# Kernel optimization log

Measured on AMD Instinct MI355X. Metric: run time of the kernel, lower is better.

## Reference

```python
import jax, jax.numpy as jnp
import numpy as np

EMBED_DIM = 1024
B, S = 8, 2048


def setup_inputs() -> dict:
    key = jax.random.key(0)
    ks = jax.random.split(key, 9)
    d = EMBED_DIM
    scale = 1.0 / np.sqrt(d)
    return {
        "x": jax.random.normal(ks[0], (B, S, d), dtype=jnp.float32),
        "Wq": jax.random.normal(ks[1], (d, d), dtype=jnp.float32) * scale,
        "bq": jnp.zeros((d,), dtype=jnp.float32),
        "Wk": jax.random.normal(ks[2], (d, d), dtype=jnp.float32) * scale,
        "bk": jnp.zeros((d,), dtype=jnp.float32),
        "Wv": jax.random.normal(ks[3], (d, d), dtype=jnp.float32) * scale,
        "bv": jnp.zeros((d,), dtype=jnp.float32),
        "ln_gamma": jnp.ones((d,), dtype=jnp.float32),
        "ln_beta": jnp.zeros((d,), dtype=jnp.float32),
    }


def _layernorm(x, gamma, beta, eps=1e-5):
    mu = jnp.mean(x, axis=-1, keepdims=True)
    var = jnp.var(x, axis=-1, keepdims=True)
    return (x - mu) * jax.lax.rsqrt(var + eps) * gamma + beta


def reference(x, Wq, bq, Wk, bk, Wv, bv, ln_gamma, ln_beta):
    # Pre-LN single-head self-attention with residual.
    # Dropout is identity (eval mode) for a deterministic reference.
    residual = x
    xn = _layernorm(x, ln_gamma, ln_beta)
    Q = jnp.einsum('bsd,de->bse', xn, Wq.T) + bq  # torch Linear: x @ W^T + b
    K = jnp.einsum('bsd,de->bse', xn, Wk.T) + bk
    V = jnp.einsum('bsd,de->bse', xn, Wv.T) + bv
    scores = jnp.einsum('bqd,bkd->bqk', Q, K) / jnp.sqrt(jnp.float32(EMBED_DIM))
    attention_weights = jax.nn.softmax(scores, axis=-1)  # [B, S, S]
    attention_output = jnp.einsum('bqk,bkd->bqd', attention_weights, V)
    output = residual + attention_output
    return (output, attention_weights)
```

## Files before the change

### kernel.cpp

```cpp
#include <hip/hip_runtime.h>

#define EMBED 1024
#define SEQ 2048
#define BATCH 8

typedef __bf16 bf16;
typedef bf16 bf16x4 __attribute__((ext_vector_type(4)));
typedef bf16 bf16x8 __attribute__((ext_vector_type(8)));
typedef float f32x4 __attribute__((ext_vector_type(4)));

__device__ __forceinline__ void async_copy16(const bf16* g, bf16* l) {
  __builtin_amdgcn_global_load_lds(
      (const __attribute__((address_space(1))) unsigned int*)g,
      (__attribute__((address_space(3))) unsigned int*)l, 16, 0, 0);
}

template <int KDEPTH, int LDA, int LDB>
__device__ __forceinline__ void gemm_core(const bf16* __restrict__ Ab,
                                          const bf16* __restrict__ Bb,
                                          bf16* lds, f32x4 (&acc)[8][4]) {
  const int tid = (int)threadIdx.x;
  const int lane = tid & 63;
  const int wid = tid >> 6;
  const int wm = wid >> 2, wn = wid & 3;
  const int c = lane & 15, g = lane >> 4;
  const int sx = c & 7;
  constexpr int NT = KDEPTH / 64;

  int srow[4], scol[4];
#pragma unroll
  for (int r = 0; r < 4; ++r) {
    int idx = r * 512 + tid;
    srow[r] = idx >> 3;
    scol[r] = ((idx & 7) ^ ((idx >> 3) & 7)) * 8;
  }

  auto stage = [&](int bufsel, int t) {
    bf16* dst = lds + bufsel * 32768;
    const int k0 = t * 64;
#pragma unroll
    for (int r = 0; r < 4; ++r)
      async_copy16(Ab + (size_t)srow[r] * LDA + k0 + scol[r], dst + (r * 512 + tid) * 8);
#pragma unroll
    for (int r = 0; r < 4; ++r)
      async_copy16(Bb + (size_t)srow[r] * LDB + k0 + scol[r], dst + 16384 + (r * 512 + tid) * 8);
  };

  stage(0, 0);
  stage(1, 1);
  asm volatile("s_waitcnt vmcnt(8)" ::: "memory");
  __builtin_amdgcn_s_barrier();
  __builtin_amdgcn_sched_barrier(0);

  const int aoffb = (wm * 128 + c) * 64;
  const int boffb = (wn * 64 + c) * 64;

  for (int t = 0; t < NT; ++t) {
    const bf16* bufA = lds + (t & 1) * 32768;
    const bf16* bufB = bufA + 16384;

    bf16x8 bfr[4][2];
#pragma unroll
    for (int ni = 0; ni < 4; ++ni)
#pragma unroll
      for (int ks = 0; ks < 2; ++ks)
        bfr[ni][ks] = *reinterpret_cast<const bf16x8*>(
            bufB + boffb + ni * 1024 + (((ks * 4 + g) ^ sx) * 8));
    __builtin_amdgcn_s_setprio(1);
#pragma unroll
    for (int p = 0; p < 4; ++p) {
      bf16x8 afr[2][2];
#pragma unroll
      for (int mm = 0; mm < 2; ++mm)
#pragma unroll
        for (int ks = 0; ks < 2; ++ks)
          afr[mm][ks] = *reinterpret_cast<const bf16x8*>(
              bufA + aoffb + (p * 2 + mm) * 1024 + (((ks * 4 + g) ^ sx) * 8));
#pragma unroll
      for (int mm = 0; mm < 2; ++mm)
#pragma unroll
        for (int ni = 0; ni < 4; ++ni)
#pragma unroll
          for (int ks = 0; ks < 2; ++ks)
            acc[p * 2 + mm][ni] = __builtin_amdgcn_mfma_f32_16x16x32_bf16(
                afr[mm][ks], bfr[ni][ks], acc[p * 2 + mm][ni], 0, 0, 0);
    }
    __builtin_amdgcn_s_setprio(0);

    __builtin_amdgcn_sched_barrier(0);
    asm volatile("s_waitcnt lgkmcnt(0)" ::: "memory");
    __builtin_amdgcn_s_barrier();
    if (t + 2 < NT) {
      stage(t & 1, t + 2);
      asm volatile("s_waitcnt vmcnt(8)" ::: "memory");
    } else {
      asm volatile("s_waitcnt vmcnt(0)" ::: "memory");
    }
    __builtin_amdgcn_s_barrier();
    __builtin_amdgcn_sched_barrier(0);
  }
}

__global__ __launch_bounds__(256) void k_pre(const float* __restrict__ x,
                                             const float* __restrict__ gamma,
                                             const float* __restrict__ beta,
                                             const float* __restrict__ wq,
                                             const float* __restrict__ wk,
                                             const float* __restrict__ wv,
                                             bf16* __restrict__ xn,
                                             bf16* __restrict__ wall) {
  const int bid = (int)blockIdx.x;
  const int tid = (int)threadIdx.x;
  if (bid >= BATCH * SEQ) {
    int i4 = (bid - BATCH * SEQ) * 256 + tid;
    int m = i4 >> 18;
    int loc = i4 & 262143;
    const float* src = (m == 0) ? wq : (m == 1) ? wk : wv;
    float4 v = reinterpret_cast<const float4*>(src)[loc];
    bf16x4 o;
    o[0] = (bf16)v.x; o[1] = (bf16)v.y; o[2] = (bf16)v.z; o[3] = (bf16)v.w;
    reinterpret_cast<bf16x4*>(wall)[i4] = o;
    return;
  }
  const int row = bid;
  const float4 v = reinterpret_cast<const float4*>(x + (size_t)row * EMBED)[tid];
  float s = v.x + v.y + v.z + v.w;
  float q = v.x * v.x + v.y * v.y + v.z * v.z + v.w * v.w;
#pragma unroll
  for (int off = 1; off < 64; off <<= 1) {
    s += __shfl_xor(s, off);
    q += __shfl_xor(q, off);
  }
  __shared__ float ls[4], lq[4];
  int w = tid >> 6;
  if ((tid & 63) == 0) { ls[w] = s; lq[w] = q; }
  __syncthreads();
  s = ls[0] + ls[1] + ls[2] + ls[3];
  q = lq[0] + lq[1] + lq[2] + lq[3];
  float mean = s * (1.0f / EMBED);
  float var = q * (1.0f / EMBED) - mean * mean;
  float rstd = rsqrtf(var + 1e-5f);
  float4 gm = reinterpret_cast<const float4*>(gamma)[tid];
  float4 b = reinterpret_cast<const float4*>(beta)[tid];
  bf16x4 o;
  o[0] = (bf16)((v.x - mean) * rstd * gm.x + b.x);
  o[1] = (bf16)((v.y - mean) * rstd * gm.y + b.y);
  o[2] = (bf16)((v.z - mean) * rstd * gm.z + b.z);
  o[3] = (bf16)((v.w - mean) * rstd * gm.w + b.w);
  reinterpret_cast<bf16x4*>(xn + (size_t)row * EMBED)[tid] = o;
}

__global__ __launch_bounds__(512) void k_qkv256(const bf16* __restrict__ xn,
                                                const bf16* __restrict__ wall,
                                                const float* __restrict__ bq,
                                                const float* __restrict__ bk,
                                                const float* __restrict__ bv,
                                                bf16* __restrict__ qbuf,
                                                bf16* __restrict__ kbuf,
                                                bf16* __restrict__ vt) {
  extern __shared__ bf16 smem[];
  const int h = (int)blockIdx.x;
  const int xcd = h & 7, pos = h >> 3;
  const int z = pos >> 5;
  const int mtile = xcd * 8 + ((pos >> 2) & 7);
  const int ntile = pos & 3;
  const int tid = (int)threadIdx.x, lane = tid & 63, wid = tid >> 6;
  const int wm = wid >> 2, wn = wid & 3;
  const int cc = lane & 15, g = lane >> 4;
  const bf16* Ab = xn + (size_t)(mtile * 256) * EMBED;
  const bf16* Bb = wall + (size_t)z * EMBED * EMBED + (size_t)(ntile * 256) * EMBED;
  f32x4 acc[8][4];
#pragma unroll
  for (int i = 0; i < 8; ++i)
#pragma unroll
    for (int j = 0; j < 4; ++j) acc[i][j] = (f32x4){0.f, 0.f, 0.f, 0.f};
  gemm_core<EMBED, EMBED, EMBED>(Ab, Bb, smem, acc);

  const int c0 = ntile * 256 + wn * 64;
  const int r0 = mtile * 256 + wm * 128;
  if (z < 2) {
    bf16* o = z ? kbuf : qbuf;
    const float* bias = z ? bk : bq;
#pragma unroll
    for (int mi = 0; mi < 8; ++mi)
#pragma unroll
      for (int ni = 0; ni < 4; ++ni) {
        int col = c0 + ni * 16 + cc;
        float bb = bias[col];
#pragma unroll
        for (int j = 0; j < 4; ++j)
          o[(size_t)(r0 + mi * 16 + g * 4 + j) * EMBED + col] = (bf16)(acc[mi][ni][j] + bb);
      }
  } else {
#pragma unroll
    for (int mi = 0; mi < 8; ++mi) {
      int srow = r0 + mi * 16 + g * 4;
      int b = srow >> 11, sl = srow & (SEQ - 1);
#pragma unroll
      for (int ni = 0; ni < 4; ++ni) {
        int col = c0 + ni * 16 + cc;
        float bb = bv[col];
        bf16x4 pk;
#pragma unroll
        for (int j = 0; j < 4; ++j) pk[j] = (bf16)(acc[mi][ni][j] + bb);
        *reinterpret_cast<bf16x4*>(vt + (size_t)b * EMBED * SEQ + (size_t)col * SEQ + sl) = pk;
      }
    }
  }
}

__global__ __launch_bounds__(512) void k_scores256(const bf16* __restrict__ qm,
                                                   const bf16* __restrict__ km,
                                                   bf16* __restrict__ wbf,
                                                   float* __restrict__ partial) {
  extern __shared__ bf16 smem[];
  const int h = (int)blockIdx.x;
  const int bb = h & 7, pos = h >> 3;
  const int mtile = pos >> 3, ntile = pos & 7;
  const int tid = (int)threadIdx.x, lane = tid & 63, wid = tid >> 6;
  const int wm = wid >> 2, wn = wid & 3;
  const int cc = lane & 15, g = lane >> 4;
  const bf16* Ab = qm + (size_t)bb * SEQ * EMBED + (size_t)(mtile * 256) * EMBED;
  const bf16* Bb = km + (size_t)bb * SEQ * EMBED + (size_t)(ntile * 256) * EMBED;
  f32x4 acc[8][4];
#pragma unroll
  for (int i = 0; i < 8; ++i)
#pragma unroll
    for (int j = 0; j < 4; ++j) acc[i][j] = (f32x4){0.f, 0.f, 0.f, 0.f};
  gemm_core<EMBED, EMBED, EMBED>(Ab, Bb, smem, acc);

  float* red = (float*)smem;
  const int c0 = ntile * 256 + wn * 64;
#pragma unroll
  for (int mi = 0; mi < 8; ++mi) {
#pragma unroll
    for (int j = 0; j < 4; ++j) {
      int lrow = wm * 128 + mi * 16 + g * 4 + j;
      size_t grow = (size_t)bb * SEQ + mtile * 256 + lrow;
      float s = 0.f;
#pragma unroll
      for (int ni = 0; ni < 4; ++ni) {
        float e = __expf(acc[mi][ni][j] * 0.03125f);
        wbf[grow * SEQ + c0 + ni * 16 + cc] = (bf16)e;
        s += e;
      }
      s += __shfl_xor(s, 1);
      s += __shfl_xor(s, 2);
      s += __shfl_xor(s, 4);
      s += __shfl_xor(s, 8);
      if (cc == 0) red[lrow * 4 + wn] = s;
    }
  }
  __syncthreads();
  if (tid < 256) {
    float l = red[tid * 4 + 0] + red[tid * 4 + 1] + red[tid * 4 + 2] + red[tid * 4 + 3];
    partial[((size_t)bb * SEQ + mtile * 256 + tid) * 8 + ntile] = l;
  }
}

__global__ __launch_bounds__(256) void k_rowsum(const float* __restrict__ partial,
                                                float* __restrict__ rinv) {
  int row = blockIdx.x * 256 + threadIdx.x;
  const float* p = partial + (size_t)row * 8;
  float l = 0.f;
#pragma unroll
  for (int i = 0; i < 8; ++i) l += p[i];
  rinv[row] = 1.0f / l;
}

__global__ __launch_bounds__(512) void k_pv256(const bf16* __restrict__ wbf,
                                               const bf16* __restrict__ vt,
                                               const float* __restrict__ rinv,
                                               const float* __restrict__ xin,
                                               float* __restrict__ outp) {
  extern __shared__ bf16 smem[];
  const int h = (int)blockIdx.x;
  const int bb = h & 7, pos = h >> 3;
  const int mtile = pos >> 2, ntile = pos & 3;
  const int tid = (int)threadIdx.x, lane = tid & 63, wid = tid >> 6;
  const int wm = wid >> 2, wn = wid & 3;
  const int cc = lane & 15, g = lane >> 4;
  const bf16* Ab = wbf + (size_t)bb * SEQ * SEQ + (size_t)(mtile * 256) * SEQ;
  const bf16* Bb = vt + (size_t)bb * EMBED * SEQ + (size_t)(ntile * 256) * SEQ;
  f32x4 acc[8][4];
#pragma unroll
  for (int i = 0; i < 8; ++i)
#pragma unroll
    for (int j = 0; j < 4; ++j) acc[i][j] = (f32x4){0.f, 0.f, 0.f, 0.f};
  gemm_core<SEQ, SEQ, SEQ>(Ab, Bb, smem, acc);

  const int c0 = ntile * 256 + wn * 64;
#pragma unroll
  for (int mi = 0; mi < 8; ++mi) {
#pragma unroll
    for (int j = 0; j < 4; ++j) {
      size_t grow = (size_t)bb * SEQ + mtile * 256 + wm * 128 + mi * 16 + g * 4 + j;
      float ri = rinv[grow];
      size_t base = grow * EMBED;
#pragma unroll
      for (int ni = 0; ni < 4; ++ni) {
        size_t off = base + c0 + ni * 16 + cc;
        outp[off] = xin[off] + acc[mi][ni][j] * ri;
      }
    }
  }
}

__global__ __launch_bounds__(256) void k_norm_bf(const bf16* __restrict__ wbf,
                                                 const float* __restrict__ rinv,
                                                 float* __restrict__ attn) {
  size_t i8 = (size_t)blockIdx.x * 256 + threadIdx.x;
  int row = (int)(i8 >> 8);
  float ri = rinv[row];
  bf16x8 v = reinterpret_cast<const bf16x8*>(wbf)[i8];
  float4 lo, hi;
  lo.x = (float)v[0] * ri; lo.y = (float)v[1] * ri;
  lo.z = (float)v[2] * ri; lo.w = (float)v[3] * ri;
  hi.x = (float)v[4] * ri; hi.y = (float)v[5] * ri;
  hi.z = (float)v[6] * ri; hi.w = (float)v[7] * ri;
  reinterpret_cast<float4*>(attn)[i8 * 2] = lo;
  reinterpret_cast<float4*>(attn)[i8 * 2 + 1] = hi;
}

extern "C" void kernel_launch(void* const* d_in, const int* in_sizes, int n_in,
                              void* d_out, int out_size, void* d_ws, size_t ws_size,
                              hipStream_t stream) {
  const float* x = (const float*)d_in[0];
  const float* Wq = (const float*)d_in[1];
  const float* bq = (const float*)d_in[2];
  const float* Wk = (const float*)d_in[3];
  const float* bk = (const float*)d_in[4];
  const float* Wv = (const float*)d_in[5];
  const float* bv = (const float*)d_in[6];
  const float* gamma = (const float*)d_in[7];
  const float* beta = (const float*)d_in[8];

  float* out = (float*)d_out;
  float* attn = out + (size_t)BATCH * SEQ * EMBED;

  bf16* qbuf = (bf16*)d_out;
  bf16* kbuf = qbuf + (size_t)BATCH * SEQ * EMBED;

  bf16* xn = (bf16*)d_ws;
  bf16* wall = xn + (size_t)BATCH * SEQ * EMBED;
  bf16* wbf = (bf16*)d_ws;
  bf16* vt = (bf16*)d_ws + (size_t)BATCH * SEQ * SEQ;
  float* partial = (float*)((char*)d_ws + 100663296ull);
  float* rinv = (float*)((char*)d_ws + 100663296ull + 524288ull);

  hipFuncSetAttribute((const void*)k_qkv256, hipFuncAttributeMaxDynamicSharedMemorySize, 131072);
  hipFuncSetAttribute((const void*)k_scores256, hipFuncAttributeMaxDynamicSharedMemorySize, 131072);
  hipFuncSetAttribute((const void*)k_pv256, hipFuncAttributeMaxDynamicSharedMemorySize, 131072);

  k_pre<<<BATCH * SEQ + 3072, 256, 0, stream>>>(x, gamma, beta, Wq, Wk, Wv, xn, wall);
  k_qkv256<<<768, 512, 131072, stream>>>(xn, wall, bq, bk, bv, qbuf, kbuf, vt);
  k_scores256<<<512, 512, 131072, stream>>>(qbuf, kbuf, wbf, partial);
  k_rowsum<<<64, 256, 0, stream>>>(partial, rinv);
  k_pv256<<<256, 512, 131072, stream>>>(wbf, vt, rinv, x, out);
  k_norm_bf<<<16384, 256, 0, stream>>>(wbf, rinv, attn);
}
```

Baseline: 309.6 us.

## Switch GEMM core to triple-buffered 32-wide K tiles with one barrier

The shared GEMM core now stages K tiles of 32 instead of 64 and rotates through three LDS buffers instead of two. The copy for tile t+2 is issued at the start of each iteration, before the MFMAs, which removes one barrier per iteration. LDS use drops from 128 KB to 96 KB per block, and the three launches request less dynamic shared memory to match. In exchange there are twice as many iterations, each with less MFMA work to hide the wait and barrier overhead.

Result: slower. 326.1 us (+5.3%).

```diff
diff --git a/kernel.cpp b/kernel.cpp
--- a/kernel.cpp
+++ b/kernel.cpp
@@ -24,80 +24,82 @@
   const int wid = tid >> 6;
   const int wm = wid >> 2, wn = wid & 3;
   const int c = lane & 15, g = lane >> 4;
-  const int sx = c & 7;
-  constexpr int NT = KDEPTH / 64;
-
-  int srow[4], scol[4];
-#pragma unroll
-  for (int r = 0; r < 4; ++r) {
+  const int sx = c & 3;
+  constexpr int NT = KDEPTH / 32;
+
+  int srow[2], scol[2];
+#pragma unroll
+  for (int r = 0; r < 2; ++r) {
     int idx = r * 512 + tid;
-    srow[r] = idx >> 3;
-    scol[r] = ((idx & 7) ^ ((idx >> 3) & 7)) * 8;
+    srow[r] = idx >> 2;
+    scol[r] = ((idx & 3) ^ ((idx >> 2) & 3)) * 8;
   }
 
   auto stage = [&](int bufsel, int t) {
-    bf16* dst = lds + bufsel * 32768;
-    const int k0 = t * 64;
-#pragma unroll
-    for (int r = 0; r < 4; ++r)
+    bf16* dst = lds + bufsel * 16384;
+    const int k0 = t * 32;
+#pragma unroll
+    for (int r = 0; r < 2; ++r)
       async_copy16(Ab + (size_t)srow[r] * LDA + k0 + scol[r], dst + (r * 512 + tid) * 8);
 #pragma unroll
-    for (int r = 0; r < 4; ++r)
-      async_copy16(Bb + (size_t)srow[r] * LDB + k0 + scol[r], dst + 16384 + (r * 512 + tid) * 8);
+    for (int r = 0; r < 2; ++r)
+      async_copy16(Bb + (size_t)srow[r] * LDB + k0 + scol[r],
+                   dst + 8192 + (r * 512 + tid) * 8);
   };
 
   stage(0, 0);
   stage(1, 1);
-  asm volatile("s_waitcnt vmcnt(8)" ::: "memory");
+  asm volatile("s_waitcnt vmcnt(4)" ::: "memory");
   __builtin_amdgcn_s_barrier();
   __builtin_amdgcn_sched_barrier(0);
 
-  const int aoffb = (wm * 128 + c) * 64;
-  const int boffb = (wn * 64 + c) * 64;
-
+  const int aoffb = (wm * 128 + c) * 32;
+  const int boffb = (wn * 64 + c) * 32;
+
+  int cur = 0;
   for (int t = 0; t < NT; ++t) {
-    const bf16* bufA = lds + (t & 1) * 32768;
-    const bf16* bufB = bufA + 16384;
-
-    bf16x8 bfr[4][2];
+    const bf16* bufA = lds + cur * 16384;
+    const bf16* bufB = bufA + 8192;
+
+    if (t + 2 < NT) {
+      int nn = cur + 2;
+      if (nn >= 3) nn -= 3;
+      stage(nn, t + 2);
+    }
+    __builtin_amdgcn_sched_barrier(0);
+
+    bf16x8 bfr[4];
 #pragma unroll
     for (int ni = 0; ni < 4; ++ni)
-#pragma unroll
-      for (int ks = 0; ks < 2; ++ks)
-        bfr[ni][ks] = *reinterpret_cast<const bf16x8*>(
-            bufB + boffb + ni * 1024 + (((ks * 4 + g) ^ sx) * 8));
+      bfr[ni] = *reinterpret_cast<const bf16x8*>(
+          bufB + boffb + ni * 512 + ((g ^ sx) * 8));
     __builtin_amdgcn_s_setprio(1);
 #pragma unroll
     for (int p = 0; p < 4; ++p) {
-      bf16x8 afr[2][2];
+      bf16x8 afr[2];
 #pragma unroll
       for (int mm = 0; mm < 2; ++mm)
-#pragma unroll
-        for (int ks = 0; ks < 2; ++ks)
-          afr[mm][ks] = *reinterpret_cast<const bf16x8*>(
-              bufA + aoffb + (p * 2 + mm) * 1024 + (((ks * 4 + g) ^ sx) * 8));
+        afr[mm] = *reinterpret_cast<const bf16x8*>(
+            bufA + aoffb + (p * 2 + mm) * 512 + ((g ^ sx) * 8));
 #pragma unroll
       for (int mm = 0; mm < 2; ++mm)
 #pragma unroll
         for (int ni = 0; ni < 4; ++ni)
-#pragma unroll
-          for (int ks = 0; ks < 2; ++ks)
-            acc[p * 2 + mm][ni] = __builtin_amdgcn_mfma_f32_16x16x32_bf16(
-                afr[mm][ks], bfr[ni][ks], acc[p * 2 + mm][ni], 0, 0, 0);
+          acc[p * 2 + mm][ni] = __builtin_amdgcn_mfma_f32_16x16x32_bf16(
+              afr[mm], bfr[ni], acc[p * 2 + mm][ni], 0, 0, 0);
     }
     __builtin_amdgcn_s_setprio(0);
 
     __builtin_amdgcn_sched_barrier(0);
     asm volatile("s_waitcnt lgkmcnt(0)" ::: "memory");
-    __builtin_amdgcn_s_barrier();
-    if (t + 2 < NT) {
-      stage(t & 1, t + 2);
-      asm volatile("s_waitcnt vmcnt(8)" ::: "memory");
-    } else {
+    if (t + 2 < NT)
+      asm volatile("s_waitcnt vmcnt(4)" ::: "memory");
+    else
       asm volatile("s_waitcnt vmcnt(0)" ::: "memory");
-    }
     __builtin_amdgcn_s_barrier();
     __builtin_amdgcn_sched_barrier(0);
+    ++cur;
+    if (cur == 3) cur = 0;
   }
 }
 
@@ -348,14 +350,14 @@
   float* partial = (float*)((char*)d_ws + 100663296ull);
   float* rinv = (float*)((char*)d_ws + 100663296ull + 524288ull);
 
-  hipFuncSetAttribute((const void*)k_qkv256, hipFuncAttributeMaxDynamicSharedMemorySize, 131072);
-  hipFuncSetAttribute((const void*)k_scores256, hipFuncAttributeMaxDynamicSharedMemorySize, 131072);
-  hipFuncSetAttribute((const void*)k_pv256, hipFuncAttributeMaxDynamicSharedMemorySize, 131072);
+  hipFuncSetAttribute((const void*)k_qkv256, hipFuncAttributeMaxDynamicSharedMemorySize, 98304);
+  hipFuncSetAttribute((const void*)k_scores256, hipFuncAttributeMaxDynamicSharedMemorySize, 98304);
+  hipFuncSetAttribute((const void*)k_pv256, hipFuncAttributeMaxDynamicSharedMemorySize, 98304);
 
   k_pre<<<BATCH * SEQ + 3072, 256, 0, stream>>>(x, gamma, beta, Wq, Wk, Wv, xn, wall);
-  k_qkv256<<<768, 512, 131072, stream>>>(xn, wall, bq, bk, bv, qbuf, kbuf, vt);
-  k_scores256<<<512, 512, 131072, stream>>>(qbuf, kbuf, wbf, partial);
+  k_qkv256<<<768, 512, 98304, stream>>>(xn, wall, bq, bk, bv, qbuf, kbuf, vt);
+  k_scores256<<<512, 512, 98304, stream>>>(qbuf, kbuf, wbf, partial);
   k_rowsum<<<64, 256, 0, stream>>>(partial, rinv);
-  k_pv256<<<256, 512, 131072, stream>>>(wbf, vt, rinv, x, out);
+  k_pv256<<<256, 512, 98304, stream>>>(wbf, vt, rinv, x, out);
   k_norm_bf<<<16384, 256, 0, stream>>>(wbf, rinv, attn);
 }
```

## Interleave next-tile async loads with MFMA phases in GEMM main loop

Applied to the files above, without the earlier changes.

Reorganizes the GEMM K-loop so the global-to-LDS copies for the next K tile are split into four pieces: two B halves and two pairs of A quarters. Each piece is issued inside one of the four MFMA sub-phases instead of in a single block between iterations. The A tile is relaid out in LDS as row-quarter chunks so each phase loads only the chunk it needs. Prefetch distance drops from two tiles to one, and waits become finer-grained vmcnt checks. The intent is to spread memory traffic across compute and shrink the stall at iteration boundaries, at the cost of more barriers per iteration and less prefetch slack.

After: 298.0 us. 3.8% less time.

```diff
diff --git a/kernel.cpp b/kernel.cpp
--- a/kernel.cpp
+++ b/kernel.cpp
@@ -27,46 +27,40 @@
   const int sx = c & 7;
   constexpr int NT = KDEPTH / 64;
 
-  int srow[4], scol[4];
-#pragma unroll
-  for (int r = 0; r < 4; ++r) {
-    int idx = r * 512 + tid;
-    srow[r] = idx >> 3;
-    scol[r] = ((idx & 7) ^ ((idx >> 3) & 7)) * 8;
-  }
-
-  auto stage = [&](int bufsel, int t) {
-    bf16* dst = lds + bufsel * 32768;
+  auto stage_B = [&](int h, int t) {
+    bf16* dst = lds + (t & 1) * 32768 + 16384 + h * 8192;
     const int k0 = t * 64;
-#pragma unroll
-    for (int r = 0; r < 4; ++r)
-      async_copy16(Ab + (size_t)srow[r] * LDA + k0 + scol[r], dst + (r * 512 + tid) * 8);
-#pragma unroll
-    for (int r = 0; r < 4; ++r)
-      async_copy16(Bb + (size_t)srow[r] * LDB + k0 + scol[r], dst + 16384 + (r * 512 + tid) * 8);
+    const bf16* src = Bb + (size_t)(h * 128) * LDB + k0;
+#pragma unroll
+    for (int r = 0; r < 2; ++r) {
+      int idx = r * 512 + tid;
+      int row = idx >> 3, slot = idx & 7;
+      async_copy16(src + (size_t)row * LDB + ((slot ^ (row & 7)) * 8), dst + idx * 8);
+    }
   };
-
-  stage(0, 0);
-  stage(1, 1);
-  asm volatile("s_waitcnt vmcnt(8)" ::: "memory");
+  auto stage_A = [&](int q, int t) {
+    bf16* dst = lds + (t & 1) * 32768 + q * 4096;
+    const int k0 = t * 64;
+    int rib = tid >> 3, slot = tid & 7;
+    int grow = q * 32 + (rib & 31) + (rib >> 5) * 128;
+    async_copy16(Ab + (size_t)grow * LDA + k0 + ((slot ^ (rib & 7)) * 8), dst + tid * 8);
+  };
+
+  stage_B(0, 0); stage_B(1, 0);
+  stage_A(0, 0); stage_A(1, 0); stage_A(2, 0); stage_A(3, 0);
+  asm volatile("s_waitcnt vmcnt(2)" ::: "memory");
   __builtin_amdgcn_s_barrier();
   __builtin_amdgcn_sched_barrier(0);
 
-  const int aoffb = (wm * 128 + c) * 64;
   const int boffb = (wn * 64 + c) * 64;
+  const int arowb = (wm * 32 + c) * 64;
 
   for (int t = 0; t < NT; ++t) {
     const bf16* bufA = lds + (t & 1) * 32768;
     const bf16* bufB = bufA + 16384;
-
+    const int nxt = t + 1;
+    const bool more = nxt < NT;
     bf16x8 bfr[4][2];
-#pragma unroll
-    for (int ni = 0; ni < 4; ++ni)
-#pragma unroll
-      for (int ks = 0; ks < 2; ++ks)
-        bfr[ni][ks] = *reinterpret_cast<const bf16x8*>(
-            bufB + boffb + ni * 1024 + (((ks * 4 + g) ^ sx) * 8));
-    __builtin_amdgcn_s_setprio(1);
 #pragma unroll
     for (int p = 0; p < 4; ++p) {
       bf16x8 afr[2][2];
@@ -75,7 +69,25 @@
 #pragma unroll
         for (int ks = 0; ks < 2; ++ks)
           afr[mm][ks] = *reinterpret_cast<const bf16x8*>(
-              bufA + aoffb + (p * 2 + mm) * 1024 + (((ks * 4 + g) ^ sx) * 8));
+              bufA + p * 4096 + arowb + mm * 1024 + (((ks * 4 + g) ^ sx) * 8));
+      if (p == 0) {
+#pragma unroll
+        for (int ni = 0; ni < 4; ++ni)
+#pragma unroll
+          for (int ks = 0; ks < 2; ++ks)
+            bfr[ni][ks] = *reinterpret_cast<const bf16x8*>(
+                bufB + boffb + ni * 1024 + (((ks * 4 + g) ^ sx) * 8));
+      }
+      if (more) {
+        if (p == 0) stage_B(0, nxt);
+        else if (p == 1) stage_B(1, nxt);
+        else if (p == 2) { stage_A(0, nxt); stage_A(1, nxt); }
+        else { stage_A(2, nxt); stage_A(3, nxt); }
+      }
+      __builtin_amdgcn_s_barrier();
+      asm volatile("s_waitcnt lgkmcnt(0)" ::: "memory");
+      __builtin_amdgcn_sched_barrier(0);
+      __builtin_amdgcn_s_setprio(1);
 #pragma unroll
       for (int mm = 0; mm < 2; ++mm)
 #pragma unroll
@@ -84,20 +96,18 @@
           for (int ks = 0; ks < 2; ++ks)
             acc[p * 2 + mm][ni] = __builtin_amdgcn_mfma_f32_16x16x32_bf16(
                 afr[mm][ks], bfr[ni][ks], acc[p * 2 + mm][ni], 0, 0, 0);
-    }
-    __builtin_amdgcn_s_setprio(0);
-
-    __builtin_amdgcn_sched_barrier(0);
-    asm volatile("s_waitcnt lgkmcnt(0)" ::: "memory");
-    __builtin_amdgcn_s_barrier();
-    if (t + 2 < NT) {
-      stage(t & 1, t + 2);
-      asm volatile("s_waitcnt vmcnt(8)" ::: "memory");
-    } else {
-      asm volatile("s_waitcnt vmcnt(0)" ::: "memory");
-    }
-    __builtin_amdgcn_s_barrier();
-    __builtin_amdgcn_sched_barrier(0);
+      __builtin_amdgcn_s_setprio(0);
+      __builtin_amdgcn_sched_barrier(0);
+      if (p == 1) {
+        if (more) asm volatile("s_waitcnt vmcnt(4)" ::: "memory");
+        else      asm volatile("s_waitcnt vmcnt(0)" ::: "memory");
+      }
+      if (p == 3) {
+        if (more) asm volatile("s_waitcnt vmcnt(2)" ::: "memory");
+        else      asm volatile("s_waitcnt vmcnt(0)" ::: "memory");
+      }
+      __builtin_amdgcn_s_barrier();
+    }
   }
 }
 
```
